# Performance work log

Measured on AMD Instinct MI355X. Metric: run time of the kernel, lower is better.

## Reference

```python
import jax, jax.numpy as jnp
import numpy as np

B, S, D_IN = 16, 1024, 1024
H, D_OUT = 16, 128

def setup_inputs() -> dict:
    key = jax.random.key(0)
    k1, k2, k3 = jax.random.split(key, 3)
    x = jax.random.normal(k1, (B, S, D_IN), dtype=jnp.float32)
    W = jax.random.normal(k2, (H, 3, D_IN, D_OUT), dtype=jnp.float32) * (1.0 / np.sqrt(D_IN))
    Wo = jax.random.normal(k3, (H * D_OUT, D_OUT), dtype=jnp.float32) * (1.0 / np.sqrt(H * D_OUT))
    return {"x": x, "W": W, "Wo": Wo}

def reference(x, W, Wo):
    # x: [B,S,D_IN], W: [H,3,D_IN,E], Wo: [H*E,E]
    E = W.shape[-1]
    q = jnp.einsum('bsd,hde->bhse', x, W[:, 0])
    k = jnp.einsum('bsd,hde->bhse', x, W[:, 1])
    v = jnp.einsum('bsd,hde->bhse', x, W[:, 2])
    # NOTE: source divides by (output_dim * 0.5), not sqrt(output_dim)
    scores = jnp.einsum('bhse,bhte->bhst', q, k) / (E * 0.5)
    attn = jax.nn.softmax(scores, axis=-1)
    o = jnp.einsum('bhst,bhte->bhse', attn, v)          # [B,H,S,E]
    o = jnp.transpose(o, (0, 2, 1, 3)).reshape(x.shape[0], x.shape[1], -1)  # concat heads
    return jnp.einsum('bsf,fe->bse', o, Wo)
```

## Files before the change

kernel.cpp:

```cpp
#include <hip/hip_runtime.h>

typedef unsigned short u16;
typedef _Float16 f16;
typedef __attribute__((ext_vector_type(8))) _Float16 half8;
typedef __attribute__((ext_vector_type(8))) short short8;
typedef __attribute__((ext_vector_type(4))) float f32x4;
typedef __attribute__((ext_vector_type(4))) float f4;
typedef __attribute__((ext_vector_type(4))) u16 u16x4;

#define B_ 16
#define S_ 1024
#define DIN_ 1024
#define H_ 16
#define E_ 128

#define EXPK 0.0225546041776533f

__device__ __forceinline__ u16 f2h(float f) {
  f16 h = (f16)f;
  return __builtin_bit_cast(u16, h);
}

__device__ __forceinline__ void gl2lds16(const u16* g, u16* l) {
  __builtin_amdgcn_global_load_lds((const __attribute__((address_space(1))) void*)g,
                                   (__attribute__((address_space(3))) void*)l, 16, 0, 0);
}

__global__ __launch_bounds__(256) void zero_f32(float* __restrict__ p) {
  int i = (blockIdx.x * 256 + threadIdx.x) * 4;
  f4 z = {0.f, 0.f, 0.f, 0.f};
  *reinterpret_cast<f4*>(p + i) = z;
}

__global__ __launch_bounds__(256) void cvt_f32_f16(const float* __restrict__ in,
                                                   u16* __restrict__ out) {
  int i = (blockIdx.x * 256 + threadIdx.x) * 4;
  f4 v = *reinterpret_cast<const f4*>(in + i);
  u16x4 o;
  o[0] = f2h(v[0]); o[1] = f2h(v[1]); o[2] = f2h(v[2]); o[3] = f2h(v[3]);
  *reinterpret_cast<u16x4*>(out + i) = o;
}

__global__ __launch_bounds__(256) void transpose_cvt(const float* __restrict__ in,
                                                     u16* __restrict__ out,
                                                     int R, int C) {
  __shared__ float tile[32][33];
  const size_t moff = (size_t)blockIdx.z * R * C;
  const float* src = in + moff;
  u16* dst = out + moff;
  int c0 = blockIdx.x * 32, r0 = blockIdx.y * 32;
  int tx = threadIdx.x & 31, ty = threadIdx.x >> 5;
#pragma unroll
  for (int i = 0; i < 32; i += 8)
    tile[ty + i][tx] = src[(size_t)(r0 + ty + i) * C + c0 + tx];
  __syncthreads();
#pragma unroll
  for (int i = 0; i < 32; i += 8)
    dst[(size_t)(c0 + ty + i) * R + r0 + tx] = f2h(tile[tx][ty + i]);
}

template<int MODE, int KSPLIT, int K>
__global__ __launch_bounds__(256) void gemm_bt(const u16* __restrict__ A,
                                               const u16* __restrict__ BT,
                                               u16* __restrict__ q, u16* __restrict__ kk,
                                               u16* __restrict__ vT, float* __restrict__ out) {
  const int tid = threadIdx.x;
  const int m0 = blockIdx.x * 128;
  const u16* Bblk = BT + (size_t)blockIdx.y * 128 * K;
  __shared__ __align__(16) u16 smem[132 * 128];
  u16* As = smem;
  u16* Bs = smem + 8192;
  const int w = tid >> 6, lane = tid & 63;
  const int quad = lane >> 4, ln = lane & 15;
  const int wr = w >> 1, wc = w & 1;

  const int kbeg = (KSPLIT > 1) ? blockIdx.z * (K / KSPLIT) : 0;
  constexpr int KLEN = K / KSPLIT;

  const int rr = lane >> 3;
  const int cc = (lane & 7) ^ rr;
  const u16* agp[4];
  const u16* bgp[4];
#pragma unroll
  for (int i = 0; i < 4; i++) {
    int row = i * 32 + w * 8 + rr;
    agp[i] = A + (size_t)(m0 + row) * K + kbeg + cc * 8;
    bgp[i] = Bblk + (size_t)row * K + kbeg + cc * 8;
  }

  int offA[4][2], offB[4][2];
#pragma unroll
  for (int mt = 0; mt < 4; mt++) {
    int row = wr * 64 + mt * 16 + ln;
#pragma unroll
    for (int k2 = 0; k2 < 2; k2++)
      offA[mt][k2] = row * 64 + (((k2 * 4 + quad) ^ (ln & 7)) * 8);
  }
#pragma unroll
  for (int nt = 0; nt < 4; nt++) {
    int row = wc * 64 + nt * 16 + ln;
#pragma unroll
    for (int k2 = 0; k2 < 2; k2++)
      offB[nt][k2] = row * 64 + (((k2 * 4 + quad) ^ (ln & 7)) * 8);
  }

  f32x4 acc[4][4];
  f32x4 zero = {0.f, 0.f, 0.f, 0.f};
#pragma unroll
  for (int mt = 0; mt < 4; mt++)
#pragma unroll
    for (int nt = 0; nt < 4; nt++) acc[mt][nt] = zero;

#pragma unroll
  for (int k0 = 0; k0 < KLEN; k0 += 64) {
    __syncthreads();
#pragma unroll
    for (int i = 0; i < 4; i++) {
      gl2lds16(agp[i] + k0, As + i * 2048 + w * 512);
      gl2lds16(bgp[i] + k0, Bs + i * 2048 + w * 512);
    }
    __syncthreads();
#pragma unroll
    for (int k2 = 0; k2 < 2; k2++) {
      half8 af[4], bfr[4];
#pragma unroll
      for (int mt = 0; mt < 4; mt++)
        af[mt] = *reinterpret_cast<const half8*>(&As[offA[mt][k2]]);
#pragma unroll
      for (int nt = 0; nt < 4; nt++)
        bfr[nt] = *reinterpret_cast<const half8*>(&Bs[offB[nt][k2]]);
#pragma unroll
      for (int mt = 0; mt < 4; mt++)
#pragma unroll
        for (int nt = 0; nt < 4; nt++)
          acc[mt][nt] = __builtin_amdgcn_mfma_f32_16x16x32_f16(af[mt], bfr[nt], acc[mt][nt], 0, 0, 0);
    }
  }

  if (MODE == 0) {
    const int h = blockIdx.y / 3, c = blockIdx.y % 3;
    if (c < 2) {
      u16* dst = (c == 0) ? q : kk;
      const float sc = (c == 0) ? EXPK : 1.0f;
#pragma unroll
      for (int mt = 0; mt < 4; mt++)
#pragma unroll
        for (int nt = 0; nt < 4; nt++)
#pragma unroll
          for (int r = 0; r < 4; r++) {
            int row = wr * 64 + mt * 16 + quad * 4 + r;
            int tok = m0 + row;
            int bb = tok >> 10, s = tok & 1023;
            int e = wc * 64 + nt * 16 + ln;
            dst[(((size_t)bb * H_ + h) * S_ + s) * E_ + e] = f2h(acc[mt][nt][r] * sc);
          }
    } else {
      __syncthreads();
#pragma unroll
      for (int mt = 0; mt < 4; mt++)
#pragma unroll
        for (int nt = 0; nt < 4; nt++)
#pragma unroll
          for (int r = 0; r < 4; r++) {
            int row = wr * 64 + mt * 16 + quad * 4 + r;
            int e = wc * 64 + nt * 16 + ln;
            smem[e * 132 + row] = f2h(acc[mt][nt][r]);
          }
      __syncthreads();
      const int bb = m0 >> 10, sbase = m0 & 1023;
      u16* vbase = vT + (((size_t)bb * H_ + h) * E_) * S_;
#pragma unroll
      for (int i = 0; i < 8; i++) {
        int e = (tid >> 4) + i * 16, s0 = (tid & 15) * 8;
        *reinterpret_cast<short8*>(&vbase[(size_t)e * S_ + sbase + s0]) =
            *reinterpret_cast<const short8*>(&smem[e * 132 + s0]);
      }
    }
  } else {
#pragma unroll
    for (int mt = 0; mt < 4; mt++)
#pragma unroll
      for (int nt = 0; nt < 4; nt++)
#pragma unroll
        for (int r = 0; r < 4; r++) {
          int row = wr * 64 + mt * 16 + quad * 4 + r;
          int e = wc * 64 + nt * 16 + ln;
          if (KSPLIT > 1)
            atomicAdd(&out[(size_t)(m0 + row) * E_ + e], acc[mt][nt][r]);
          else
            out[(size_t)(m0 + row) * E_ + e] = acc[mt][nt][r];
        }
  }
}

struct SmemKVP {
  u16 ks[64 * 128];
  u16 vs[128 * 64];
  u16 ps[128 * 68];
};
union SmemAttn {
  u16 qs[128 * 132];
  SmemKVP s;
};

__global__ __launch_bounds__(256, 3) void attn_kernel(const u16* __restrict__ qg,
                                                      const u16* __restrict__ kg,
                                                      const u16* __restrict__ vg,
                                                      u16* __restrict__ og) {
  __shared__ __align__(16) SmemAttn sm;
  const int tid = threadIdx.x;
  const int id = blockIdx.x;
  const int g = id >> 6, qt = (id >> 3) & 7, x = id & 7;
  const int hb = g * 8 + x;
  const int b = hb >> 4, h = hb & 15;
  const int q0 = qt * 128;
  const size_t bh = (size_t)(b * H_ + h);
  const u16* qp = qg + bh * S_ * E_;
  const u16* kp = kg + bh * S_ * E_;
  const u16* vp = vg + bh * E_ * S_;
  const int w = tid >> 6, lane = tid & 63, quad = lane >> 4, ln = lane & 15;

#pragma unroll
  for (int i = 0; i < 8; i++) {
    int idx = tid + i * 256;
    int row = idx >> 4, col = (idx & 15) * 8;
    *reinterpret_cast<short8*>(&sm.qs[row * 132 + col]) =
        *reinterpret_cast<const short8*>(&qp[(size_t)(q0 + row) * E_ + col]);
  }
  __syncthreads();
  half8 qf[2][4];
#pragma unroll
  for (int mt = 0; mt < 2; mt++)
#pragma unroll
    for (int ks = 0; ks < 4; ks++)
      qf[mt][ks] = *reinterpret_cast<const half8*>(
          &sm.qs[(w * 32 + mt * 16 + ln) * 132 + ks * 32 + quad * 8]);

  const int krow = w * 4 + (lane >> 4);
  const int kc = ((lane & 15) & 8) | (((lane & 15) & 7) ^ (krow & 7));
  const u16* kbase = kp + (size_t)krow * E_ + kc * 8;
  const int vrow = w * 8 + (lane >> 3);
  const int vc = (lane & 7) ^ ((lane >> 3) & 7);
  const u16* vbase = vp + (size_t)vrow * S_ + vc * 8;

  f32x4 zero = {0.f, 0.f, 0.f, 0.f};
  f32x4 oa[2][8];
#pragma unroll
  for (int mt = 0; mt < 2; mt++)
#pragma unroll
    for (int nt = 0; nt < 8; nt++) oa[mt][nt] = zero;
  float lsum[2][4];
#pragma unroll
  for (int mt = 0; mt < 2; mt++)
#pragma unroll
    for (int r = 0; r < 4; r++) lsum[mt][r] = 0.f;

  for (int kt = 0; kt < 16; kt++) {
    __syncthreads();
#pragma unroll
    for (int i = 0; i < 4; i++) {
      gl2lds16(kbase + (size_t)kt * 8192 + i * 16 * E_, &sm.s.ks[(i * 256 + w * 64) * 8]);
      gl2lds16(vbase + (size_t)kt * 64 + i * 32 * S_,   &sm.s.vs[(i * 256 + w * 64) * 8]);
    }
    __syncthreads();

    f32x4 sa[2][4];
#pragma unroll
    for (int mt = 0; mt < 2; mt++)
#pragma unroll
      for (int nt = 0; nt < 4; nt++) sa[mt][nt] = zero;
#pragma unroll
    for (int ks = 0; ks < 4; ks++) {
      half8 kf[4];
#pragma unroll
      for (int nt = 0; nt < 4; nt++) {
        int c = ks * 4 + quad;
        int cs = (c & 8) | ((c & 7) ^ (ln & 7));
        kf[nt] = *reinterpret_cast<const half8*>(&sm.s.ks[(nt * 16 + ln) * 128 + cs * 8]);
      }
#pragma unroll
      for (int mt = 0; mt < 2; mt++)
#pragma unroll
        for (int nt = 0; nt < 4; nt++)
          sa[mt][nt] = __builtin_amdgcn_mfma_f32_16x16x32_f16(qf[mt][ks], kf[nt], sa[mt][nt], 0, 0, 0);
    }

#pragma unroll
    for (int mt = 0; mt < 2; mt++) {
#pragma unroll
      for (int r = 0; r < 4; r++) {
        int prow = (w * 32 + mt * 16 + quad * 4 + r) * 68;
        float psum = 0.f;
#pragma unroll
        for (int nt = 0; nt < 4; nt++) {
          float p = exp2f(sa[mt][nt][r]);
          psum += p;
          sm.s.ps[prow + nt * 16 + ln] = f2h(p);
        }
        lsum[mt][r] += psum;
      }
    }

#pragma unroll
    for (int k2 = 0; k2 < 2; k2++) {
      half8 pf[2];
#pragma unroll
      for (int mt = 0; mt < 2; mt++)
        pf[mt] = *reinterpret_cast<const half8*>(
            &sm.s.ps[(w * 32 + mt * 16 + ln) * 68 + k2 * 32 + quad * 8]);
#pragma unroll
      for (int nt8 = 0; nt8 < 8; nt8++) {
        int c = k2 * 4 + quad;
        int cs = c ^ (ln & 7);
        half8 vf = *reinterpret_cast<const half8*>(&sm.s.vs[(nt8 * 16 + ln) * 64 + cs * 8]);
#pragma unroll
        for (int mt = 0; mt < 2; mt++)
          oa[mt][nt8] = __builtin_amdgcn_mfma_f32_16x16x32_f16(pf[mt], vf, oa[mt][nt8], 0, 0, 0);
      }
    }
  }

#pragma unroll
  for (int mt = 0; mt < 2; mt++) {
#pragma unroll
    for (int r = 0; r < 4; r++) {
      float l = lsum[mt][r];
#pragma unroll
      for (int d = 1; d < 16; d <<= 1) l += __shfl_xor(l, d);
      float rl = 1.0f / l;
      int srow = q0 + w * 32 + mt * 16 + quad * 4 + r;
      size_t base = ((size_t)b * S_ + srow) * (H_ * E_) + (size_t)h * E_;
#pragma unroll
      for (int nt8 = 0; nt8 < 8; nt8++)
        og[base + nt8 * 16 + ln] = f2h(oa[mt][nt8][r] * rl);
    }
  }
}

extern "C" void kernel_launch(void* const* d_in, const int* in_sizes, int n_in,
                              void* d_out, int out_size, void* d_ws, size_t ws_size,
                              hipStream_t stream) {
  const float* x = (const float*)d_in[0];
  const float* W = (const float*)d_in[1];
  const float* Wo = (const float*)d_in[2];
  float* out = (float*)d_out;
  char* ws = (char*)d_ws;

  const size_t WBT_BYTES = (size_t)H_ * 3 * DIN_ * E_ * 2;
  const size_t WOT_BYTES = (size_t)H_ * E_ * E_ * 2 * 2;
  const size_t FIXED = WBT_BYTES + WOT_BYTES;

  const size_t XB_PER   = (size_t)S_ * DIN_ * 2;
  const size_t QKV_PER  = (size_t)H_ * S_ * E_ * 2;
  const size_t OB_PER   = (size_t)S_ * H_ * E_ * 2;
  const size_t PER_ITEM = XB_PER + 3 * QKV_PER + OB_PER;

  int Bc = 1;
  for (int c = 16; c >= 1; c >>= 1) {
    if (FIXED + (size_t)c * PER_ITEM <= ws_size) { Bc = c; break; }
  }

  u16* WbT = (u16*)(ws);
  u16* WoT = (u16*)(ws + WBT_BYTES);
  char* cb = ws + FIXED;
  u16* xb  = (u16*)(cb);
  u16* qb  = (u16*)(cb + (size_t)Bc * XB_PER);
  u16* kb  = (u16*)(cb + (size_t)Bc * (XB_PER + QKV_PER));
  u16* vTb = (u16*)(cb + (size_t)Bc * (XB_PER + 2 * QKV_PER));
  u16* ob  = (u16*)(cb + (size_t)Bc * (XB_PER + 3 * QKV_PER));

  zero_f32<<<out_size / 1024, 256, 0, stream>>>(out);
  transpose_cvt<<<dim3(4, 32, 48), 256, 0, stream>>>(W, WbT, DIN_, E_);
  transpose_cvt<<<dim3(4, 64, 1), 256, 0, stream>>>(Wo, WoT, H_ * E_, E_);

  for (int b0 = 0; b0 < B_; b0 += Bc) {
    const float* xc = x + (size_t)b0 * S_ * DIN_;
    cvt_f32_f16<<<Bc * S_ * DIN_ / 1024, 256, 0, stream>>>(xc, xb);
    gemm_bt<0, 1, DIN_><<<dim3(Bc * 8, 48), 256, 0, stream>>>(xb, WbT, qb, kb, vTb, nullptr);
    attn_kernel<<<Bc * 128, 256, 0, stream>>>(qb, kb, vTb, ob);
    gemm_bt<1, 4, H_ * E_><<<dim3(Bc * 8, 1, 4), 256, 0, stream>>>(ob, WoT, nullptr, nullptr,
                                                                   nullptr, out + (size_t)b0 * S_ * E_);
  }
}
```

Before: 564.2 us.

## Keep attention probabilities in registers by computing transposed scores

```diff
diff --git a/kernel.cpp b/kernel.cpp
--- a/kernel.cpp
+++ b/kernel.cpp
@@ -164,7 +164,8 @@
           for (int r = 0; r < 4; r++) {
             int row = wr * 64 + mt * 16 + quad * 4 + r;
             int e = wc * 64 + nt * 16 + ln;
-            smem[e * 132 + row] = f2h(acc[mt][nt][r]);
+            int srow = (row & 0x60) | ((row & 12) << 1) | ((row & 16) >> 2) | (row & 3);
+            smem[e * 132 + srow] = f2h(acc[mt][nt][r]);
           }
       __syncthreads();
       const int bb = m0 >> 10, sbase = m0 & 1023;
@@ -193,14 +194,13 @@
   }
 }
 
-struct SmemKVP {
+struct SmemKV {
   u16 ks[64 * 128];
   u16 vs[128 * 64];
-  u16 ps[128 * 68];
 };
 union SmemAttn {
   u16 qs[128 * 132];
-  SmemKVP s;
+  SmemKV s;
 };
 
 __global__ __launch_bounds__(256, 3) void attn_kernel(const u16* __restrict__ qg,
@@ -249,11 +249,7 @@
   for (int mt = 0; mt < 2; mt++)
 #pragma unroll
     for (int nt = 0; nt < 8; nt++) oa[mt][nt] = zero;
-  float lsum[2][4];
-#pragma unroll
-  for (int mt = 0; mt < 2; mt++)
-#pragma unroll
-    for (int r = 0; r < 4; r++) lsum[mt][r] = 0.f;
+  float lsum[2] = {0.f, 0.f};
 
   for (int kt = 0; kt < 16; kt++) {
     __syncthreads();
@@ -282,32 +278,31 @@
       for (int mt = 0; mt < 2; mt++)
 #pragma unroll
         for (int nt = 0; nt < 4; nt++)
-          sa[mt][nt] = __builtin_amdgcn_mfma_f32_16x16x32_f16(qf[mt][ks], kf[nt], sa[mt][nt], 0, 0, 0);
-    }
-
+          sa[mt][nt] = __builtin_amdgcn_mfma_f32_16x16x32_f16(kf[nt], qf[mt][ks], sa[mt][nt], 0, 0, 0);
+    }
+
+    half8 pfr[2][2];
 #pragma unroll
     for (int mt = 0; mt < 2; mt++) {
-#pragma unroll
-      for (int r = 0; r < 4; r++) {
-        int prow = (w * 32 + mt * 16 + quad * 4 + r) * 68;
-        float psum = 0.f;
-#pragma unroll
-        for (int nt = 0; nt < 4; nt++) {
-          float p = exp2f(sa[mt][nt][r]);
-          psum += p;
-          sm.s.ps[prow + nt * 16 + ln] = f2h(p);
-        }
-        lsum[mt][r] += psum;
+      float psum = 0.f;
+#pragma unroll
+      for (int k2 = 0; k2 < 2; k2++) {
+        half8 ph;
+#pragma unroll
+        for (int hhalf = 0; hhalf < 2; hhalf++)
+#pragma unroll
+          for (int r = 0; r < 4; r++) {
+            float p = exp2f(sa[mt][k2 * 2 + hhalf][r]);
+            psum += p;
+            ph[hhalf * 4 + r] = (f16)p;
+          }
+        pfr[mt][k2] = ph;
       }
+      lsum[mt] += psum;
     }
 
 #pragma unroll
     for (int k2 = 0; k2 < 2; k2++) {
-      half8 pf[2];
-#pragma unroll
-      for (int mt = 0; mt < 2; mt++)
-        pf[mt] = *reinterpret_cast<const half8*>(
-            &sm.s.ps[(w * 32 + mt * 16 + ln) * 68 + k2 * 32 + quad * 8]);
 #pragma unroll
       for (int nt8 = 0; nt8 < 8; nt8++) {
         int c = k2 * 4 + quad;
@@ -315,19 +310,20 @@
         half8 vf = *reinterpret_cast<const half8*>(&sm.s.vs[(nt8 * 16 + ln) * 64 + cs * 8]);
 #pragma unroll
         for (int mt = 0; mt < 2; mt++)
-          oa[mt][nt8] = __builtin_amdgcn_mfma_f32_16x16x32_f16(pf[mt], vf, oa[mt][nt8], 0, 0, 0);
+          oa[mt][nt8] = __builtin_amdgcn_mfma_f32_16x16x32_f16(pfr[mt][k2], vf, oa[mt][nt8], 0, 0, 0);
       }
     }
   }
 
 #pragma unroll
   for (int mt = 0; mt < 2; mt++) {
+    float l = lsum[mt];
+    l += __shfl_xor(l, 16);
+    l += __shfl_xor(l, 32);
 #pragma unroll
     for (int r = 0; r < 4; r++) {
-      float l = lsum[mt][r];
-#pragma unroll
-      for (int d = 1; d < 16; d <<= 1) l += __shfl_xor(l, d);
-      float rl = 1.0f / l;
+      float lr = __shfl(l, quad * 4 + r);
+      float rl = 1.0f / lr;
       int srow = q0 + w * 32 + mt * 16 + quad * 4 + r;
       size_t base = ((size_t)b * S_ + srow) * (H_ * E_) + (size_t)h * E_;
 #pragma unroll
```

Measured after the change: 556.0 us. No clear change (-1.5%).
